# Kernel tuning notes

Hardware: AMD Instinct MI355X
Metric: run time of the kernel (lower is better)

Reference implementation:

```python
import jax, jax.numpy as jnp
import numpy as np


def setup_inputs() -> dict:
    key = jax.random.key(0)
    k1, k2, k3, k4 = jax.random.split(key, 4)
    B, T, d_model, d_internal = 4, 2048, 1024, 64
    x = jax.random.normal(k1, (B, T, d_model), dtype=jnp.float32)
    # torch.nn.Linear weights: [out_features, in_features]
    s = 1.0 / np.sqrt(d_model)
    W_Q = jax.random.uniform(k2, (d_internal, d_model), jnp.float32, -s, s)
    W_K = jax.random.uniform(k3, (d_internal, d_model), jnp.float32, -s, s)
    W_V = jax.random.uniform(k4, (d_internal, d_model), jnp.float32, -s, s)
    return {"x": x, "W_Q": W_Q, "W_K": W_K, "W_V": W_V}


def reference(x, W_Q, W_K, W_V):
    B, T, C = x.shape  # C == d_model
    Q = jnp.einsum('btc,dc->btd', x, W_Q)
    K = jnp.einsum('btc,dc->btd', x, W_K)
    # Faithful to source bug: V is computed with W_K, W_V is unused.
    V = jnp.einsum('btc,dc->btd', x, W_K)
    scale = C ** (-0.5)  # source scales by d_model, not d_internal
    attn = jnp.einsum('btd,bsd->bts', Q, K) * scale  # [B,T,T]
    causal = jnp.tril(jnp.ones((T, T), dtype=bool))
    attn = jnp.where(causal[None, :, :], attn, -jnp.inf)
    attn = jax.nn.softmax(attn, axis=-1)
    return jnp.einsum('bts,bsd->btd', attn, V)
```

## Files before the change

kernel.cpp:

```cpp
#include <hip/hip_runtime.h>
#include <hip/hip_bf16.h>
#include <cstdint>
#include <cstddef>

#define BB 4
#define TT 2048
#define DM 1024
#define DH 64

typedef __attribute__((ext_vector_type(8))) short short8;
typedef __attribute__((ext_vector_type(4))) float floatx4;

__device__ __forceinline__ unsigned short f2bf(float f) {
    union { float f; unsigned int u; } v; v.f = f;
    unsigned int u = v.u;
    u += 0x7fffu + ((u >> 16) & 1u);
    return (unsigned short)(u >> 16);
}

__device__ __forceinline__ float bf2f(unsigned short h) {
    union { unsigned int u; float f; } v;
    v.u = ((unsigned int)h) << 16;
    return v.f;
}

__device__ __forceinline__ unsigned int cvtpk(float a, float b) {
    unsigned int r;
    asm("v_cvt_pk_bf16_f32 %0, %1, %2" : "=v"(r) : "v"(a), "v"(b));
    return r;
}

__device__ __forceinline__ short8 cvt8(float4 lo, float4 hi) {
    union { unsigned int u[4]; short8 s; } v;
    v.u[0] = cvtpk(lo.x, lo.y);
    v.u[1] = cvtpk(lo.z, lo.w);
    v.u[2] = cvtpk(hi.x, hi.y);
    v.u[3] = cvtpk(hi.z, hi.w);
    return v.s;
}

#define WTHREADS (8 * 32 * 64)

__global__ __launch_bounds__(256) void wtile_kernel(const float* __restrict__ wq,
                                                    const float* __restrict__ wk,
                                                    unsigned short* __restrict__ wbt) {
    const int j  = blockIdx.x * 256 + threadIdx.x;
    const int l  = j & 63;
    const int kc = (j >> 6) & 31;
    const int nt = j >> 11;
    const float* wbase = (nt < 4) ? wq : wk;
    const float* src = wbase + (size_t)((nt & 3) * 16 + (l & 15)) * DM
                             + kc * 32 + (l >> 4) * 8;
    float4 a = *reinterpret_cast<const float4*>(src);
    float4 b = *reinterpret_cast<const float4*>(src + 4);
    *reinterpret_cast<short8*>(wbt + (size_t)j * 8) = cvt8(a, b);
}

__global__ __launch_bounds__(256) void proj_kernel(const float* __restrict__ x,
                                                   const unsigned short* __restrict__ wbt,
                                                   unsigned short* __restrict__ qo,
                                                   unsigned short* __restrict__ ko,
                                                   unsigned short* __restrict__ kt) {
    __shared__ __align__(16) unsigned short sA[2][16 * 64 * 8];

    const int tid  = threadIdx.x;
    const int wave = tid >> 6;
    const int lane = tid & 63;
    const int col  = lane & 15;
    const int quad = lane >> 4;
    const int mt   = blockIdx.x;

    const float* xtile = x + (size_t)mt * 16 * DM;
    const unsigned short* bq = wbt + ((size_t)wave * 32 * 64) * 8;
    const unsigned short* bk = wbt + ((size_t)(4 + wave) * 32 * 64) * 8;

    floatx4 accQ = (floatx4){0.f, 0.f, 0.f, 0.f};
    floatx4 accK = (floatx4){0.f, 0.f, 0.f, 0.f};

#pragma unroll 4
    for (int i = 0; i < 4; ++i) {
        const int e  = tid + i * 256;
        const int kc = e >> 6;
        const int l  = e & 63;
        const float* src = xtile + (size_t)(l & 15) * DM + kc * 32 + (l >> 4) * 8;
        float4 a = *reinterpret_cast<const float4*>(src);
        float4 b = *reinterpret_cast<const float4*>(src + 4);
        *reinterpret_cast<short8*>(sA[0] + (size_t)e * 8) = cvt8(a, b);
    }
    __syncthreads();

    float4 h1a[4], h1b[4];
#pragma unroll 4
    for (int i = 0; i < 4; ++i) {
        const int e  = tid + i * 256;
        const int kc = 16 + (e >> 6);
        const int l  = e & 63;
        const float* src = xtile + (size_t)(l & 15) * DM + kc * 32 + (l >> 4) * 8;
        h1a[i] = *reinterpret_cast<const float4*>(src);
        h1b[i] = *reinterpret_cast<const float4*>(src + 4);
    }

#pragma unroll
    for (int kc = 0; kc < 16; ++kc) {
        short8 a  = *reinterpret_cast<const short8*>(sA[0] + ((size_t)kc * 64 + lane) * 8);
        short8 b0 = *reinterpret_cast<const short8*>(bq + ((size_t)kc * 64 + lane) * 8);
        short8 b1 = *reinterpret_cast<const short8*>(bk + ((size_t)kc * 64 + lane) * 8);
        accQ = __builtin_amdgcn_mfma_f32_16x16x32_bf16(a, b0, accQ, 0, 0, 0);
        accK = __builtin_amdgcn_mfma_f32_16x16x32_bf16(a, b1, accK, 0, 0, 0);
    }

#pragma unroll 4
    for (int i = 0; i < 4; ++i) {
        const int e = tid + i * 256;
        *reinterpret_cast<short8*>(sA[1] + (size_t)e * 8) = cvt8(h1a[i], h1b[i]);
    }
    __syncthreads();

#pragma unroll
    for (int kc = 0; kc < 16; ++kc) {
        short8 a  = *reinterpret_cast<const short8*>(sA[1] + ((size_t)kc * 64 + lane) * 8);
        short8 b0 = *reinterpret_cast<const short8*>(bq + ((size_t)(16 + kc) * 64 + lane) * 8);
        short8 b1 = *reinterpret_cast<const short8*>(bk + ((size_t)(16 + kc) * 64 + lane) * 8);
        accQ = __builtin_amdgcn_mfma_f32_16x16x32_bf16(a, b0, accQ, 0, 0, 0);
        accK = __builtin_amdgcn_mfma_f32_16x16x32_bf16(a, b1, accK, 0, 0, 0);
    }

    const int g = wave * 16 + col;
    unsigned short hk[4];
#pragma unroll
    for (int r = 0; r < 4; ++r) {
        const size_t row = (size_t)(mt * 16 + quad * 4 + r);
        qo[row * DH + g] = f2bf(accQ[r] * 0.04508422f);
        hk[r] = f2bf(accK[r]);
        ko[row * DH + g] = hk[r];
    }

    __syncthreads();
    unsigned short* kts = (unsigned short*)sA;
#pragma unroll
    for (int r = 0; r < 4; ++r)
        kts[g * 16 + quad * 4 + r] = hk[r];
    __syncthreads();
    if (tid < 128) {
        const int d  = tid >> 1;
        const int s8 = (tid & 1) * 8;
        const int b4 = mt >> 7;
        const int s0 = (mt & 127) * 16 + s8;
        short8 v = *reinterpret_cast<const short8*>(kts + d * 16 + s8);
        *reinterpret_cast<short8*>(kt + ((size_t)(b4 * 64 + d)) * TT + s0) = v;
    }
}

__global__ __launch_bounds__(512) void flash_kernel(const unsigned short* __restrict__ qb,
                                                    const unsigned short* __restrict__ kb,
                                                    const unsigned short* __restrict__ ktb,
                                                    float* __restrict__ out) {
    const int h = blockIdx.x & 1;
    const int p = (blockIdx.x >> 1) & 31;
    const int b = blockIdx.x >> 6;

    const int qtA = p, qtB = 63 - p;
    const int q0A = qtA * 32, q0B = qtB * 32;

    __shared__ __align__(16) unsigned short Pl[8][4][16][40];
    __shared__ __align__(16) float Ored[2][16][68];
    __shared__ float lred[2][16];

    const int tid  = threadIdx.x;
    const int wv   = tid >> 6;
    const int lane = tid & 63;
    const int col  = lane & 15;
    const int quad = lane >> 4;

    {
        float* z = &Ored[0][0][0];
        for (int i = tid; i < 2 * 16 * 68; i += 512) z[i] = 0.f;
        if (tid < 32) lred[tid >> 4][tid & 15] = 0.f;
    }
    __syncthreads();

    const unsigned short* kp  = kb  + (size_t)b * TT * DH;
    const unsigned short* ktp = ktb + (size_t)b * 64 * TT;
    const int qrowA = q0A + h * 16, qrowB = q0B + h * 16;
    const unsigned short* qpA = qb + ((size_t)b * TT + qrowA) * DH;
    const unsigned short* qpB = qb + ((size_t)b * TT + qrowB) * DH;

    short8 qfA0 = *reinterpret_cast<const short8*>(qpA + (size_t)col * DH + quad * 8);
    short8 qfA1 = *reinterpret_cast<const short8*>(qpA + (size_t)col * DH + 32 + quad * 8);
    short8 qfB0 = *reinterpret_cast<const short8*>(qpB + (size_t)col * DH + quad * 8);
    short8 qfB1 = *reinterpret_cast<const short8*>(qpB + (size_t)col * DH + 32 + quad * 8);

    const int w0 = (65 * wv) >> 3;
    const int w1 = (65 * (wv + 1)) >> 3;

    floatx4 oA[4], oB[4];
#pragma unroll
    for (int t = 0; t < 4; ++t) { oA[t] = (floatx4){0.f,0.f,0.f,0.f}; oB[t] = (floatx4){0.f,0.f,0.f,0.f}; }
    float lrowA[4] = {0.f,0.f,0.f,0.f}, lrowB[4] = {0.f,0.f,0.f,0.f};

    auto body = [&](int s0, int slot, bool domask, const short8& qf0, const short8& qf1,
                    int qrow, floatx4* o, float* lrow) {
        float sv[2][4];
#pragma unroll
        for (int st = 0; st < 2; ++st) {
            const int skey = s0 + 2 * col + st;
            const unsigned short* kr = kp + (size_t)skey * DH + quad * 8;
            short8 kf0 = *reinterpret_cast<const short8*>(kr);
            short8 kf1 = *reinterpret_cast<const short8*>(kr + 32);
            floatx4 z = (floatx4){0.f, 0.f, 0.f, 0.f};
            z = __builtin_amdgcn_mfma_f32_16x16x32_bf16(qf0, kf0, z, 0, 0, 0);
            z = __builtin_amdgcn_mfma_f32_16x16x32_bf16(qf1, kf1, z, 0, 0, 0);
#pragma unroll
            for (int r = 0; r < 4; ++r) {
                float pv = __builtin_exp2f(z[r]);
                if (domask) pv = (skey <= qrow + quad * 4 + r) ? pv : 0.f;
                sv[st][r] = pv;
                lrow[r] += pv;
            }
        }
#pragma unroll
        for (int r = 0; r < 4; ++r) {
            unsigned int* prow = reinterpret_cast<unsigned int*>(&Pl[wv][slot][quad * 4 + r][0]);
            prow[col] = cvtpk(sv[0][r], sv[1][r]);
        }
        short8 pf = *reinterpret_cast<const short8*>(&Pl[wv][slot][col][quad * 8]);

#pragma unroll
        for (int t = 0; t < 4; ++t) {
            short8 vf = *reinterpret_cast<const short8*>(
                ktp + (size_t)(t * 16 + col) * TT + s0 + quad * 8);
            o[t] = __builtin_amdgcn_mfma_f32_16x16x32_bf16(pf, vf, o[t], 0, 0, 0);
        }
    };

    const int a_end = min(w1, p + 1);
    for (int j = w0; j < a_end; ++j)
        body(32 * j, j & 3, j == qtA, qfA0, qfA1, qrowA, oA, lrowA);

    const int b_beg = max(w0, p + 1);
    for (int j = b_beg; j < w1; ++j) {
        const int i = j - p - 1;
        body(32 * i, j & 3, i == qtB, qfB0, qfB1, qrowB, oB, lrowB);
    }

#pragma unroll
    for (int m = 1; m < 16; m <<= 1)
#pragma unroll
        for (int r = 0; r < 4; ++r) {
            lrowA[r] += __shfl_xor(lrowA[r], m, 64);
            lrowB[r] += __shfl_xor(lrowB[r], m, 64);
        }

    if (w0 < p + 1) {
#pragma unroll
        for (int t = 0; t < 4; ++t)
#pragma unroll
            for (int r = 0; r < 4; ++r)
                atomicAdd(&Ored[0][quad * 4 + r][t * 16 + col], oA[t][r]);
        if (col == 0)
#pragma unroll
            for (int r = 0; r < 4; ++r)
                atomicAdd(&lred[0][quad * 4 + r], lrowA[r]);
    }
    if (w1 > p + 1) {
#pragma unroll
        for (int t = 0; t < 4; ++t)
#pragma unroll
            for (int r = 0; r < 4; ++r)
                atomicAdd(&Ored[1][quad * 4 + r][t * 16 + col], oB[t][r]);
        if (col == 0)
#pragma unroll
            for (int r = 0; r < 4; ++r)
                atomicAdd(&lred[1][quad * 4 + r], lrowB[r]);
    }
    __syncthreads();

    {
        const int tile = tid >> 8;
        const int row  = (tid >> 4) & 15;
        const int c4   = (tid & 15) * 4;
        const float inv = 1.0f / lred[tile][row];
        const int grow = (tile == 0 ? qrowA : qrowB) + row;
        float4 r = {Ored[tile][row][c4 + 0] * inv, Ored[tile][row][c4 + 1] * inv,
                    Ored[tile][row][c4 + 2] * inv, Ored[tile][row][c4 + 3] * inv};
        *reinterpret_cast<float4*>(out + ((size_t)b * TT + grow) * DH + c4) = r;
    }
}

extern "C" void kernel_launch(void* const* d_in, const int* in_sizes, int n_in,
                              void* d_out, int out_size, void* d_ws, size_t ws_size,
                              hipStream_t stream) {
    const float* x  = (const float*)d_in[0];
    const float* wq = (const float*)d_in[1];
    const float* wk = (const float*)d_in[2];

    unsigned short* wbt = (unsigned short*)d_ws;
    unsigned short* qo  = wbt + (size_t)WTHREADS * 8;
    unsigned short* ko  = qo + (size_t)BB * TT * DH;
    unsigned short* kt  = ko + (size_t)BB * TT * DH;
    float* out = (float*)d_out;

    hipLaunchKernelGGL(wtile_kernel, dim3(WTHREADS / 256), dim3(256), 0, stream, wq, wk, wbt);
    hipLaunchKernelGGL(proj_kernel,  dim3((BB * TT) / 16), dim3(256), 0, stream, x, wbt, qo, ko, kt);
    hipLaunchKernelGGL(flash_kernel, dim3(BB * 64),        dim3(512), 0, stream, qo, ko, kt, out);
}
```

Measured before the change: 116.7 us.

## Compute transposed scores so P feeds PV MFMA from registers

Swaps the MFMA operand order to compute S^T (keys as rows, queries as columns) and permutes which keys each lane loads. The exponentiated probabilities then land in registers already laid out as the A operand of the PV MFMA. This removes the per-tile LDS round-trip for P and shrinks the row-sum reduction to two cross-lane shuffles. The risk is that the key-permutation and mask indexing must match the MFMA layouts exactly.

```diff
diff --git a/kernel.cpp b/kernel.cpp
--- a/kernel.cpp
+++ b/kernel.cpp
@@ -162,7 +162,6 @@
     const int qtA = p, qtB = 63 - p;
     const int q0A = qtA * 32, q0B = qtB * 32;
 
-    __shared__ __align__(16) unsigned short Pl[8][4][16][40];
     __shared__ __align__(16) float Ored[2][16][68];
     __shared__ float lred[2][16];
 
@@ -196,60 +195,60 @@
     floatx4 oA[4], oB[4];
 #pragma unroll
     for (int t = 0; t < 4; ++t) { oA[t] = (floatx4){0.f,0.f,0.f,0.f}; oB[t] = (floatx4){0.f,0.f,0.f,0.f}; }
-    float lrowA[4] = {0.f,0.f,0.f,0.f}, lrowB[4] = {0.f,0.f,0.f,0.f};
-
-    auto body = [&](int s0, int slot, bool domask, const short8& qf0, const short8& qf1,
-                    int qrow, floatx4* o, float* lrow) {
+    float lsumA = 0.f, lsumB = 0.f;
+
+    const int koff0 = ((lane >> 2) & 3) * 8 + (lane & 3);
+
+    auto body = [&](int s0, bool domask, const short8& qf0, const short8& qf1,
+                    int qrow, floatx4* o, float& lsum) {
+        const int qglob = qrow + col;
         float sv[2][4];
 #pragma unroll
         for (int st = 0; st < 2; ++st) {
-            const int skey = s0 + 2 * col + st;
+            const int skey = s0 + koff0 + st * 4;
             const unsigned short* kr = kp + (size_t)skey * DH + quad * 8;
             short8 kf0 = *reinterpret_cast<const short8*>(kr);
             short8 kf1 = *reinterpret_cast<const short8*>(kr + 32);
             floatx4 z = (floatx4){0.f, 0.f, 0.f, 0.f};
-            z = __builtin_amdgcn_mfma_f32_16x16x32_bf16(qf0, kf0, z, 0, 0, 0);
-            z = __builtin_amdgcn_mfma_f32_16x16x32_bf16(qf1, kf1, z, 0, 0, 0);
+            z = __builtin_amdgcn_mfma_f32_16x16x32_bf16(kf0, qf0, z, 0, 0, 0);
+            z = __builtin_amdgcn_mfma_f32_16x16x32_bf16(kf1, qf1, z, 0, 0, 0);
+            const int kbase = s0 + quad * 8 + st * 4;
 #pragma unroll
             for (int r = 0; r < 4; ++r) {
                 float pv = __builtin_exp2f(z[r]);
-                if (domask) pv = (skey <= qrow + quad * 4 + r) ? pv : 0.f;
+                if (domask) pv = (kbase + r <= qglob) ? pv : 0.f;
                 sv[st][r] = pv;
-                lrow[r] += pv;
+                lsum += pv;
             }
         }
-#pragma unroll
-        for (int r = 0; r < 4; ++r) {
-            unsigned int* prow = reinterpret_cast<unsigned int*>(&Pl[wv][slot][quad * 4 + r][0]);
-            prow[col] = cvtpk(sv[0][r], sv[1][r]);
-        }
-        short8 pf = *reinterpret_cast<const short8*>(&Pl[wv][slot][col][quad * 8]);
+        union { unsigned int u[4]; short8 s; } pa;
+        pa.u[0] = cvtpk(sv[0][0], sv[0][1]);
+        pa.u[1] = cvtpk(sv[0][2], sv[0][3]);
+        pa.u[2] = cvtpk(sv[1][0], sv[1][1]);
+        pa.u[3] = cvtpk(sv[1][2], sv[1][3]);
 
 #pragma unroll
         for (int t = 0; t < 4; ++t) {
             short8 vf = *reinterpret_cast<const short8*>(
                 ktp + (size_t)(t * 16 + col) * TT + s0 + quad * 8);
-            o[t] = __builtin_amdgcn_mfma_f32_16x16x32_bf16(pf, vf, o[t], 0, 0, 0);
+            o[t] = __builtin_amdgcn_mfma_f32_16x16x32_bf16(pa.s, vf, o[t], 0, 0, 0);
         }
     };
 
     const int a_end = min(w1, p + 1);
     for (int j = w0; j < a_end; ++j)
-        body(32 * j, j & 3, j == qtA, qfA0, qfA1, qrowA, oA, lrowA);
+        body(32 * j, j == qtA, qfA0, qfA1, qrowA, oA, lsumA);
 
     const int b_beg = max(w0, p + 1);
     for (int j = b_beg; j < w1; ++j) {
         const int i = j - p - 1;
-        body(32 * i, j & 3, i == qtB, qfB0, qfB1, qrowB, oB, lrowB);
-    }
-
-#pragma unroll
-    for (int m = 1; m < 16; m <<= 1)
-#pragma unroll
-        for (int r = 0; r < 4; ++r) {
-            lrowA[r] += __shfl_xor(lrowA[r], m, 64);
-            lrowB[r] += __shfl_xor(lrowB[r], m, 64);
-        }
+        body(32 * i, i == qtB, qfB0, qfB1, qrowB, oB, lsumB);
+    }
+
+    lsumA += __shfl_xor(lsumA, 16, 64);
+    lsumA += __shfl_xor(lsumA, 32, 64);
+    lsumB += __shfl_xor(lsumB, 16, 64);
+    lsumB += __shfl_xor(lsumB, 32, 64);
 
     if (w0 < p + 1) {
 #pragma unroll
@@ -257,10 +256,7 @@
 #pragma unroll
             for (int r = 0; r < 4; ++r)
                 atomicAdd(&Ored[0][quad * 4 + r][t * 16 + col], oA[t][r]);
-        if (col == 0)
-#pragma unroll
-            for (int r = 0; r < 4; ++r)
-                atomicAdd(&lred[0][quad * 4 + r], lrowA[r]);
+        if (lane < 16) atomicAdd(&lred[0][lane], lsumA);
     }
     if (w1 > p + 1) {
 #pragma unroll
@@ -268,10 +264,7 @@
 #pragma unroll
             for (int r = 0; r < 4; ++r)
                 atomicAdd(&Ored[1][quad * 4 + r][t * 16 + col], oB[t][r]);
-        if (col == 0)
-#pragma unroll
-            for (int r = 0; r < 4; ++r)
-                atomicAdd(&lred[1][quad * 4 + r], lrowB[r]);
+        if (lane < 16) atomicAdd(&lred[1][lane], lsumB);
     }
     __syncthreads();
 
```

After: 116.1 us (median of 2 runs). About the same (-0.5%).
